# Optimization experiments

Hardware: AMD Instinct MI355X
Metric: run time of the kernel (lower is better)

Reference implementation:

```python
import jax, jax.numpy as jnp
import numpy as np

H_DIM = 2048
D_FF = 4 * H_DIM
NUM_EXPERTS = 8
NUM_SHARED = 2
BATCH, SEQ = 2, 2048


def setup_inputs() -> dict:
    key = jax.random.key(0)
    ks = jax.random.split(key, 10)
    s = 0.02
    return {
        "x": jax.random.normal(ks[0], (BATCH, SEQ, H_DIM), dtype=jnp.float32),
        "ws_w1": jax.random.normal(ks[1], (NUM_SHARED, H_DIM, D_FF), dtype=jnp.float32) * s,
        "ws_b1": jnp.zeros((NUM_SHARED, D_FF), dtype=jnp.float32),
        "ws_w2": jax.random.normal(ks[2], (NUM_SHARED, D_FF, H_DIM), dtype=jnp.float32) * s,
        "ws_b2": jnp.zeros((NUM_SHARED, H_DIM), dtype=jnp.float32),
        "we_w1": jax.random.normal(ks[3], (NUM_EXPERTS, H_DIM, D_FF), dtype=jnp.float32) * s,
        "we_b1": jnp.zeros((NUM_EXPERTS, D_FF), dtype=jnp.float32),
        "we_w2": jax.random.normal(ks[4], (NUM_EXPERTS, D_FF, H_DIM), dtype=jnp.float32) * s,
        "we_b2": jnp.zeros((NUM_EXPERTS, H_DIM), dtype=jnp.float32),
        "wg": jax.random.normal(ks[5], (H_DIM, NUM_EXPERTS), dtype=jnp.float32) * s,
        "top_k": 2,
    }


def reference(x, ws_w1, ws_b1, ws_w2, ws_b2, we_w1, we_b1, we_w2, we_b2, wg, top_k):
    B, S, D = x.shape
    xt = x.reshape(-1, D)  # [T, D], T = B*S
    T = xt.shape[0]

    # ---- shared experts: sum over NUM_SHARED dense MLPs ----
    hs = jax.nn.relu(jnp.einsum('td,ndf->ntf', xt, ws_w1) + ws_b1[:, None, :])
    shared = jnp.einsum('ntf,nfd->td', hs, ws_w2) + ws_b2.sum(axis=0)  # [T, D]

    # ---- sparse top-k routed MoE ----
    logits = xt @ wg                       # [T, E] router logits
    probs = jax.nn.softmax(logits, axis=-1)
    topv, topi = jax.lax.top_k(probs, top_k)
    gates = jnp.zeros_like(probs).at[jnp.arange(T)[:, None], topi].set(topv)  # [T, E]

    moe = jnp.zeros_like(xt)
    for e in range(we_w1.shape[0]):  # small fixed expert count
        he = jax.nn.relu(xt @ we_w1[e] + we_b1[e])
        ye = he @ we_w2[e] + we_b2[e]
        moe = moe + gates[:, e:e + 1] * ye

    out = (shared + moe).reshape(B, S, D)
    return out, logits
```

## Files before the change

### kernel.cpp

```cpp
#include <hip/hip_runtime.h>

#define TOKENS 4096
#define HD 2048
#define FF 8192
#define NE 8
#define NS 2

typedef __attribute__((ext_vector_type(8))) short bf16x8;
typedef __attribute__((ext_vector_type(4))) float f32x4;

__device__ __forceinline__ unsigned rnd_bf(unsigned u) {
  return u + 0x7fffu + ((u >> 16) & 1u);
}
__device__ __forceinline__ unsigned short f2bf(float f) {
  unsigned u = __builtin_bit_cast(unsigned, f);
  return (unsigned short)(rnd_bf(u) >> 16);
}

#define GLDS16(gp, lp)                                                         \
  __builtin_amdgcn_global_load_lds(                                            \
      (const __attribute__((address_space(1))) unsigned*)(const void*)(gp),    \
      (__attribute__((address_space(3))) unsigned*)(lp), 16, 0, 0)

__global__ void router_kernel(const float* __restrict__ x, const float* __restrict__ wg,
                              float* __restrict__ logits_out, int* __restrict__ topi,
                              float* __restrict__ topv, int* __restrict__ counts,
                              unsigned short* __restrict__ xb) {
  const int wave = threadIdx.x >> 6, lane = threadIdx.x & 63;
  const int t = blockIdx.x * 4 + wave;
  const float* xr = x + (size_t)t * HD;
  unsigned short* xbr = xb + (size_t)t * HD;
  float acc[8];
#pragma unroll
  for (int e = 0; e < 8; ++e) acc[e] = 0.f;
  for (int d = lane; d < HD; d += 64) {
    const float xv = xr[d];
    xbr[d] = f2bf(xv);
    const float4 w0 = *(const float4*)(wg + (size_t)d * 8);
    const float4 w1 = *(const float4*)(wg + (size_t)d * 8 + 4);
    acc[0] += xv * w0.x; acc[1] += xv * w0.y; acc[2] += xv * w0.z; acc[3] += xv * w0.w;
    acc[4] += xv * w1.x; acc[5] += xv * w1.y; acc[6] += xv * w1.z; acc[7] += xv * w1.w;
  }
#pragma unroll
  for (int e = 0; e < 8; ++e) {
#pragma unroll
    for (int off = 32; off > 0; off >>= 1) acc[e] += __shfl_xor(acc[e], off);
  }
  if (lane == 0) {
    *(float4*)(logits_out + (size_t)t * 8)     = make_float4(acc[0], acc[1], acc[2], acc[3]);
    *(float4*)(logits_out + (size_t)t * 8 + 4) = make_float4(acc[4], acc[5], acc[6], acc[7]);
    float mx = acc[0];
#pragma unroll
    for (int e = 1; e < 8; ++e) mx = fmaxf(mx, acc[e]);
    float p[8], s = 0.f;
#pragma unroll
    for (int e = 0; e < 8; ++e) { p[e] = expf(acc[e] - mx); s += p[e]; }
    const float inv = 1.f / s;
    int i1 = 0;
#pragma unroll
    for (int e = 1; e < 8; ++e) if (acc[e] > acc[i1]) i1 = e;
    int i2 = (i1 == 0) ? 1 : 0;
#pragma unroll
    for (int e = 0; e < 8; ++e) if (e != i1 && acc[e] > acc[i2]) i2 = e;
    topi[2 * t]     = i1; topv[2 * t]     = p[i1] * inv;
    topi[2 * t + 1] = i2; topv[2 * t + 1] = p[i2] * inv;
    atomicAdd(&counts[i1], 1);
    atomicAdd(&counts[i2], 1);
  }
}

__global__ void offs_kernel(const int* __restrict__ counts, int* __restrict__ offs,
                            int* __restrict__ cursors) {
  if (threadIdx.x == 0) {
    int r = 0;
    for (int e = 0; e < NE; ++e) { offs[e] = r; cursors[e] = r; r += counts[e]; }
  }
}

__global__ void gather_kernel(const unsigned short* __restrict__ xb,
                              const int* __restrict__ topi, const float* __restrict__ topv,
                              int* __restrict__ cursors, unsigned short* __restrict__ xg,
                              int* __restrict__ row_token, float* __restrict__ row_gate,
                              int* __restrict__ row_of) {
  const int wave = threadIdx.x >> 6, lane = threadIdx.x & 63;
  const int t = blockIdx.x * 4 + wave;
  const uint4* src = (const uint4*)(xb + (size_t)t * HD);
#pragma unroll
  for (int j = 0; j < 2; ++j) {
    const int e = topi[2 * t + j];
    int pos = 0;
    if (lane == 0) {
      pos = atomicAdd(&cursors[e], 1);
      row_token[pos] = t;
      row_gate[pos] = topv[2 * t + j];
      row_of[2 * t + j] = pos;
    }
    pos = __shfl(pos, 0);
    uint4* dst = (uint4*)(xg + (size_t)pos * HD);
#pragma unroll
    for (int c = lane; c < 256; c += 64) dst[c] = src[c];
  }
}

template <int K, int N>
__global__ __launch_bounds__(256) void pack_wt(const float* __restrict__ we,
                                               const float* __restrict__ ws,
                                               unsigned short* __restrict__ dstw) {
  const int e = blockIdx.z;
  const float* src = (e < NE) ? (we + (size_t)e * K * N) : (ws + (size_t)(e - NE) * K * N);
  unsigned short* dst = dstw + (size_t)e * K * N;
  const int nt = blockIdx.x * 64;
  const int kt = blockIdx.y * 64;
  __shared__ unsigned short t[64][73];
  const int tid = threadIdx.x;
  const int rr = tid >> 4, cc = (tid & 15) * 4;
#pragma unroll
  for (int i = 0; i < 4; ++i) {
    const int k = rr + i * 16;
    float4 v = *(const float4*)(src + (size_t)(kt + k) * N + nt + cc);
    t[k][cc + 0] = f2bf(v.x);
    t[k][cc + 1] = f2bf(v.y);
    t[k][cc + 2] = f2bf(v.z);
    t[k][cc + 3] = f2bf(v.w);
  }
  __syncthreads();
  const int nr = tid >> 2, kc = (tid & 3) * 16;
  unsigned u[8];
#pragma unroll
  for (int j = 0; j < 8; ++j)
    u[j] = (unsigned)t[kc + 2 * j][nr] | ((unsigned)t[kc + 2 * j + 1][nr] << 16);
  unsigned short* dp = dst + (size_t)(nt + nr) * K + kt + kc;
  uint4 v0; v0.x = u[0]; v0.y = u[1]; v0.z = u[2]; v0.w = u[3];
  uint4 v1; v1.x = u[4]; v1.y = u[5]; v1.z = u[6]; v1.w = u[7];
  *(uint4*)dp = v0;
  *(uint4*)(dp + 8) = v1;
}

template <int MS>
__device__ __forceinline__ void rd_a(bf16x8 (&d)[8], const unsigned short* base,
                                     int wr, int fr, int fq, int swz) {
#pragma unroll
  for (int mi = 0; mi < 4; ++mi)
#pragma unroll
    for (int ks = 0; ks < 2; ++ks)
      d[mi * 2 + ks] = *(const bf16x8*)(base + (wr * 128 + MS * 64 + mi * 16 + fr) * 64 +
                                        (((ks * 4 + fq) ^ swz) << 3));
}
template <int NSUB>
__device__ __forceinline__ void rd_b(bf16x8 (&d)[4], const unsigned short* base,
                                     int wc, int fr, int fq, int swz) {
#pragma unroll
  for (int ni = 0; ni < 2; ++ni)
#pragma unroll
    for (int ks = 0; ks < 2; ++ks)
      d[ni * 2 + ks] = *(const bf16x8*)(base + (wc * 64 + NSUB * 32 + ni * 16 + fr) * 64 +
                                        (((ks * 4 + fq) ^ swz) << 3));
}
template <int MS, int NSUB>
__device__ __forceinline__ void mm16(f32x4 (&acc)[8][4], const bf16x8 (&a)[8],
                                     const bf16x8 (&b)[4]) {
  __builtin_amdgcn_s_setprio(1);
#pragma unroll
  for (int mi = 0; mi < 4; ++mi)
#pragma unroll
    for (int ni = 0; ni < 2; ++ni)
#pragma unroll
      for (int ks = 0; ks < 2; ++ks)
        acc[MS * 4 + mi][NSUB * 2 + ni] = __builtin_amdgcn_mfma_f32_16x16x32_bf16(
            a[mi * 2 + ks], b[ni * 2 + ks], acc[MS * 4 + mi][NSUB * 2 + ni], 0, 0, 0);
  __builtin_amdgcn_s_setprio(0);
}

template <int K>
__device__ __forceinline__ void kloop(
    const unsigned short* __restrict__ A, const unsigned short* __restrict__ A2,
    const unsigned short* __restrict__ Bt, const unsigned short* __restrict__ Bt2,
    int ksw, unsigned short* smem, int m0, int n0, f32x4 (&acc)[8][4],
    int wr, int wc, int fr, int fq, int swz,
    int wrA, int wcB, int lr8, int lc8, int scol, int nkt) {
#define SAK(s, kt, b)                                                          \
  { int kl_ = (kt); const unsigned short* ab_ = A;                             \
    if (kl_ >= ksw) { ab_ = A2; kl_ -= ksw; }                                  \
    const int r0_ = wrA + (s) * 64 + lr8;                                      \
    const unsigned short* s_ = ab_ + (size_t)(m0 + r0_) * K + kl_ * 64 + scol; \
    unsigned short* d_ = smem + (b) * 32768 + r0_ * 64 + lc8 * 8;              \
    GLDS16(s_, d_); GLDS16(s_ + (size_t)8 * K, d_ + 8 * 64); }
#define SBK(s, kt, b)                                                          \
  { int kl_ = (kt); const unsigned short* bb_ = Bt;                            \
    if (kl_ >= ksw) { bb_ = Bt2; kl_ -= ksw; }                                 \
    const int r0_ = wcB + (s) * 32 + lr8;                                      \
    const unsigned short* s_ = bb_ + (size_t)(n0 + r0_) * K + kl_ * 64 + scol; \
    unsigned short* d_ = smem + (b) * 32768 + 16384 + r0_ * 64 + lc8 * 8;      \
    GLDS16(s_, d_); GLDS16(s_ + (size_t)8 * K, d_ + 8 * 64); }

  SAK(0, 0, 0); SAK(1, 0, 0); SBK(0, 0, 0); SBK(1, 0, 0);
  SAK(0, 1, 1); SAK(1, 1, 1); SBK(0, 1, 1); SBK(1, 1, 1);
  asm volatile("s_waitcnt vmcnt(8)" ::: "memory");
  __builtin_amdgcn_s_barrier();

  bf16x8 a0[8], a1[8], b0[4], b1[4];
  rd_a<0>(a0, smem, wr, fr, fq, swz);
  rd_b<0>(b0, smem + 16384, wc, fr, fq, swz);

  for (int t = 0; t < nkt; ++t) {
    const int cur = t & 1;
    const int tp2 = (t + 2 < nkt) ? t + 2 : t;
    const unsigned short* As_c = smem + cur * 32768;
    const unsigned short* Bs_c = As_c + 16384;
    const unsigned short* As_n = smem + (cur ^ 1) * 32768;
    const unsigned short* Bs_n = As_n + 16384;
    rd_b<1>(b1, Bs_c, wc, fr, fq, swz);
    mm16<0, 0>(acc, a0, b0);
    rd_a<1>(a1, As_c, wr, fr, fq, swz);
    mm16<0, 1>(acc, a0, b1);
    asm volatile("s_waitcnt lgkmcnt(0)" ::: "memory");
    __builtin_amdgcn_s_barrier();
    __builtin_amdgcn_sched_barrier(0);
    SAK(0, tp2, cur); SBK(0, tp2, cur);
    mm16<1, 0>(acc, a1, b0);
    asm volatile("s_waitcnt vmcnt(4)" ::: "memory");
    __builtin_amdgcn_s_barrier();
    __builtin_amdgcn_sched_barrier(0);
    rd_a<0>(a0, As_n, wr, fr, fq, swz);
    rd_b<0>(b0, Bs_n, wc, fr, fq, swz);
    SAK(1, tp2, cur); SBK(1, tp2, cur);
    mm16<1, 1>(acc, a1, b1);
  }
#undef SAK
#undef SBK
}

__global__ __launch_bounds__(512, 2) void g1k(
    const unsigned short* __restrict__ Ash, const unsigned short* __restrict__ Art,
    const unsigned short* __restrict__ wt1,
    const float* __restrict__ bE, const float* __restrict__ bS,
    unsigned short* __restrict__ hout,
    const int* __restrict__ counts, const int* __restrict__ offs,
    int do_pack, const float* __restrict__ we_w2, const float* __restrict__ ws_w2,
    unsigned short* __restrict__ wt2) {
  constexpr int K = HD;
  constexpr int NBX = FF / 256;
  constexpr int NWG = NBX * 16;
  extern __shared__ unsigned short smem[];

  const int e = blockIdx.z;
  int M;
  const unsigned short* A;
  const float* bias;
  int hbase;
  if (e < NE) {
    M = counts[e];
    A = Art + (size_t)offs[e] * K;
    bias = bE + (size_t)e * FF;
    hbase = offs[e];
  } else {
    M = TOKENS;
    A = Ash;
    bias = bS + (size_t)(e - NE) * FF;
    hbase = 2 * TOKENS + (e - NE) * TOKENS;
  }
  const unsigned short* Bt = wt1 + (size_t)e * HD * FF;

  int flat = blockIdx.x + NBX * blockIdx.y;
  flat = (flat & 7) * (NWG >> 3) + (flat >> 3);
  const int m0 = (flat & 15) * 256;
  const int n0 = (flat >> 4) * 256;
  const int tid = threadIdx.x;

  if (m0 >= M) {
    if (!do_pack) return;
    int total = 0, prefix = 0;
    for (int e2 = 0; e2 < NE; ++e2) {
      int mb = (counts[e2] + 255) >> 8; if (mb > 16) mb = 16;
      const int inv = 32 * (16 - mb);
      if (e2 < e) prefix += inv;
      total += inv;
    }
    int mb_e = (counts[e] + 255) >> 8; if (mb_e > 16) mb_e = 16;
    const int m_idx = flat & 15, n_idx = flat >> 4;
    const int rank = prefix + n_idx * (16 - mb_e) + (m_idx - mb_e);
    unsigned short* ps = smem;
    const int NT = 10 * 128 * 32;
    const int kk = tid >> 3, cc = (tid & 7) * 8;
    float4 r0a, r0b;
    int i = rank;
    if (i < NT) {
      const int e2 = i >> 12, rem = i & 4095, ktt = rem >> 5, ntt = rem & 31;
      const float* src = (e2 < NE) ? (we_w2 + (size_t)e2 * FF * HD)
                                   : (ws_w2 + (size_t)(e2 - NE) * FF * HD);
      const float* sp = src + (size_t)(ktt * 64 + kk) * HD + ntt * 64 + cc;
      r0a = *(const float4*)sp; r0b = *(const float4*)(sp + 4);
    }
    int it = 0;
    while (i < NT) {
      const int inext = i + total;
      float4 r1a, r1b;
      if (inext < NT) {
        const int e2 = inext >> 12, rem = inext & 4095, ktt = rem >> 5, ntt = rem & 31;
        const float* src = (e2 < NE) ? (we_w2 + (size_t)e2 * FF * HD)
                                     : (ws_w2 + (size_t)(e2 - NE) * FF * HD);
        const float* sp = src + (size_t)(ktt * 64 + kk) * HD + ntt * 64 + cc;
        r1a = *(const float4*)sp; r1b = *(const float4*)(sp + 4);
      }
      unsigned short* pb = ps + (it & 1) * (64 * 73);
      {
        unsigned short* tp = pb + kk * 73 + cc;
        tp[0] = f2bf(r0a.x); tp[1] = f2bf(r0a.y); tp[2] = f2bf(r0a.z); tp[3] = f2bf(r0a.w);
        tp[4] = f2bf(r0b.x); tp[5] = f2bf(r0b.y); tp[6] = f2bf(r0b.z); tp[7] = f2bf(r0b.w);
      }
      __syncthreads();
      {
        const int e2 = i >> 12, rem = i & 4095, ktt = rem >> 5, ntt = rem & 31;
        unsigned short* dst = wt2 + (size_t)e2 * HD * FF;
        const int nn = tid >> 3, kc = (tid & 7) * 8;
        unsigned u[4];
#pragma unroll
        for (int j = 0; j < 4; ++j)
          u[j] = (unsigned)pb[(kc + 2 * j) * 73 + nn] |
                 ((unsigned)pb[(kc + 2 * j + 1) * 73 + nn] << 16);
        uint4 v; v.x = u[0]; v.y = u[1]; v.z = u[2]; v.w = u[3];
        *(uint4*)(dst + (size_t)(ntt * 64 + nn) * FF + ktt * 64 + kc) = v;
      }
      r0a = r1a; r0b = r1b;
      i = inext; ++it;
    }
    return;
  }

  const int wid = tid >> 6, ln = tid & 63;
  const int wr = wid >> 2, wc = wid & 3;
  const int fr = ln & 15, fq = ln >> 4;
  const int swz = fr & 7;
  const int lr8 = ln >> 3;
  const int lc8 = ln & 7;
  const int scol = (lc8 ^ lr8) << 3;
  const int wrA = wr * 128 + wc * 16;
  const int wcB = wc * 64 + wr * 16;

  f32x4 acc[8][4];
#pragma unroll
  for (int i = 0; i < 8; ++i)
#pragma unroll
    for (int j = 0; j < 4; ++j) acc[i][j] = (f32x4){0.f, 0.f, 0.f, 0.f};

  kloop<K>(A, A, Bt, Bt, 1 << 30, smem, m0, n0, acc, wr, wc, fr, fq, swz,
           wrA, wcB, lr8, lc8, scol, K / 64);

#pragma unroll
  for (int nn = 0; nn < 4; ++nn) {
#pragma unroll
    for (int mm = 0; mm < 8; ++mm) {
      const int col = n0 + wc * 64 + (nn >> 1) * 32 + (nn & 1) * 16 + fr;
      const float bb = bias[col];
#pragma unroll
      for (int j = 0; j < 4; ++j) {
        const int r = m0 + wr * 128 + (mm >> 2) * 64 + (mm & 3) * 16 + fq * 4 + j;
        if (r < M) {
          float v = acc[mm][nn][j] + bb;
          v = v > 0.f ? v : 0.f;
          hout[(size_t)(hbase + r) * FF + col] = f2bf(v);
        }
      }
    }
  }
}

__global__ __launch_bounds__(512, 2) void g2k(
    const unsigned short* __restrict__ hbuf, const unsigned short* __restrict__ wt2,
    const float* __restrict__ bE, const float* __restrict__ bS,
    float* __restrict__ ybuf,
    const int* __restrict__ counts, const int* __restrict__ offs) {
  constexpr int K = FF;
  constexpr int NBX = HD / 256;
  constexpr int NWG = NBX * 16;
  extern __shared__ unsigned short smem[];

  const int e = blockIdx.z;
  const bool merged = (e == NE);
  int M, nkt, ksw, hbase;
  const unsigned short *A, *A2, *B, *B2;
  const float *bias, *bias2;
  if (!merged) {
    M = counts[e];
    A = hbuf + (size_t)offs[e] * K;  A2 = A;
    B = wt2 + (size_t)e * HD * FF;   B2 = B;
    bias = bE + (size_t)e * HD;      bias2 = nullptr;
    hbase = offs[e];
    nkt = 128; ksw = 1 << 30;
  } else {
    M = TOKENS;
    A  = hbuf + (size_t)(2 * TOKENS) * K;
    A2 = hbuf + (size_t)(3 * TOKENS) * K;
    B  = wt2 + (size_t)NE * HD * FF;
    B2 = wt2 + (size_t)(NE + 1) * HD * FF;
    bias = bS;  bias2 = bS + HD;
    hbase = 2 * TOKENS;
    nkt = 256; ksw = 128;
  }

  int flat = blockIdx.x + NBX * blockIdx.y;
  flat = (flat & 7) * (NWG >> 3) + (flat >> 3);
  const int m0 = (flat & 15) * 256;
  const int n0 = (flat >> 4) * 256;
  if (m0 >= M) return;

  const int tid = threadIdx.x;
  const int wid = tid >> 6, ln = tid & 63;
  const int wr = wid >> 2, wc = wid & 3;
  const int fr = ln & 15, fq = ln >> 4;
  const int swz = fr & 7;
  const int lr8 = ln >> 3;
  const int lc8 = ln & 7;
  const int scol = (lc8 ^ lr8) << 3;
  const int wrA = wr * 128 + wc * 16;
  const int wcB = wc * 64 + wr * 16;

  f32x4 acc[8][4];
#pragma unroll
  for (int i = 0; i < 8; ++i)
#pragma unroll
    for (int j = 0; j < 4; ++j) acc[i][j] = (f32x4){0.f, 0.f, 0.f, 0.f};

  kloop<K>(A, A2, B, B2, ksw, smem, m0, n0, acc, wr, wc, fr, fq, swz,
           wrA, wcB, lr8, lc8, scol, nkt);

#pragma unroll
  for (int nn = 0; nn < 4; ++nn) {
#pragma unroll
    for (int mm = 0; mm < 8; ++mm) {
      const int colw = wc * 64 + (nn >> 1) * 32 + (nn & 1) * 16 + fr;
      float bb = bias[n0 + colw];
      if (merged) bb += bias2[n0 + colw];
#pragma unroll
      for (int j = 0; j < 4; ++j) {
        const int r = m0 + wr * 128 + (mm >> 2) * 64 + (mm & 3) * 16 + fq * 4 + j;
        if (r < M)
          ybuf[(size_t)(hbase + r) * HD + n0 + colw] = acc[mm][nn][j] + bb;
      }
    }
  }
}

__global__ __launch_bounds__(256) void reduce_kernel(
    const float* __restrict__ ybuf, const int* __restrict__ row_of,
    const float* __restrict__ topv, float* __restrict__ out) {
  const int t = blockIdx.x;
  const int d = threadIdx.x * 8;
  const float g0 = topv[2 * t], g1 = topv[2 * t + 1];
  const float* y0 = ybuf + (size_t)row_of[2 * t] * HD + d;
  const float* y1 = ybuf + (size_t)row_of[2 * t + 1] * HD + d;
  const float* s0 = ybuf + (size_t)(2 * TOKENS + t) * HD + d;
  float* o = out + (size_t)t * HD + d;
#pragma unroll
  for (int q = 0; q < 2; ++q) {
    const float4 a = *(const float4*)(s0 + q * 4);
    const float4 c = *(const float4*)(y0 + q * 4);
    const float4 e = *(const float4*)(y1 + q * 4);
    float4 r;
    r.x = a.x + g0 * c.x + g1 * e.x;
    r.y = a.y + g0 * c.y + g1 * e.y;
    r.z = a.z + g0 * c.z + g1 * e.z;
    r.w = a.w + g0 * c.w + g1 * e.w;
    *(float4*)(o + q * 4) = r;
  }
}

extern "C" void kernel_launch(void* const* d_in, const int* in_sizes, int n_in,
                              void* d_out, int out_size, void* d_ws, size_t ws_size,
                              hipStream_t stream) {
  const float* x     = (const float*)d_in[0];
  const float* ws_w1 = (const float*)d_in[1];
  const float* ws_b1 = (const float*)d_in[2];
  const float* ws_w2 = (const float*)d_in[3];
  const float* ws_b2 = (const float*)d_in[4];
  const float* we_w1 = (const float*)d_in[5];
  const float* we_b1 = (const float*)d_in[6];
  const float* we_w2 = (const float*)d_in[7];
  const float* we_b2 = (const float*)d_in[8];
  const float* wg    = (const float*)d_in[9];

  float* out = (float*)d_out;
  float* logits = out + (size_t)TOKENS * HD;

  hipFuncSetAttribute(reinterpret_cast<const void*>(g1k),
                      hipFuncAttributeMaxDynamicSharedMemorySize, 131072);
  hipFuncSetAttribute(reinterpret_cast<const void*>(g2k),
                      hipFuncAttributeMaxDynamicSharedMemorySize, 131072);

  char* ws = (char*)d_ws;
  unsigned short* wt1  = (unsigned short*)ws;
  unsigned short* wt2  = (unsigned short*)(ws + 335544320);
  unsigned short* xb   = (unsigned short*)(ws + 671088640);
  unsigned short* xg   = (unsigned short*)(ws + 687865856);
  unsigned short* hbuf = (unsigned short*)(ws + 721944576);
  char* ctrl = ws + 990380032;
  float* ybuf = (float*)ws;
  int*   row_token = (int*)(ctrl);
  float* row_gate  = (float*)(ctrl + 32768);
  int*   topi      = (int*)(ctrl + 65536);
  float* topv      = (float*)(ctrl + 98304);
  int*   counts    = (int*)(ctrl + 131072);
  int*   offs      = (int*)(ctrl + 131104);
  int*   cursors   = (int*)(ctrl + 131136);
  int*   row_of    = (int*)(ctrl + 131168);

  hipMemsetAsync(counts, 0, NE * sizeof(int), stream);
  router_kernel<<<1024, 256, 0, stream>>>(x, wg, logits, topi, topv, counts, xb);
  offs_kernel<<<1, 64, 0, stream>>>(counts, offs, cursors);
  gather_kernel<<<1024, 256, 0, stream>>>(xb, topi, topv, cursors, xg,
                                          row_token, row_gate, row_of);
  pack_wt<HD, FF><<<dim3(FF / 64, HD / 64, 10), 256, 0, stream>>>(we_w1, ws_w1, wt1);
  g1k<<<dim3(32, 16, 10), 512, 131072, stream>>>(
      xb, xg, wt1, we_b1, ws_b1, hbuf, counts, offs, 1, we_w2, ws_w2, wt2);
  g2k<<<dim3(8, 16, 9), 512, 131072, stream>>>(
      hbuf, wt2, we_b2, ws_b2, ybuf, counts, offs);
  reduce_kernel<<<TOKENS, 256, 0, stream>>>(ybuf, row_of, topv, out);

  (void)in_sizes; (void)n_in; (void)out_size; (void)ws_size;
}
```

Measured before the change: 1.861 ms.

## Restructure GEMM k-loop into 8-phase ping-pong schedule with per-phase barriers

Replaces the double-buffered k-loop with an unrolled two-tile, eight-phase schedule. Each MFMA cluster is bracketed by workgroup barriers, and the LDS reads and global-to-LDS loads are interleaved between phases so that the waves alternate compute and memory work. The aim is to hide LDS and global load latency behind MFMA, in the style of a ping-pong between the two waves per SIMD. It adds many more barriers and tighter waitcnt accounting, and it assumes nkt is even.

```diff
diff --git a/kernel.cpp b/kernel.cpp
--- a/kernel.cpp
+++ b/kernel.cpp
@@ -171,8 +171,17 @@
   __builtin_amdgcn_s_setprio(0);
 }
 
+#define PH_BAR_PRE()                                                           \
+  __builtin_amdgcn_sched_barrier(0);                                           \
+  __builtin_amdgcn_s_barrier();                                                \
+  asm volatile("s_waitcnt lgkmcnt(0)" ::: "memory");                           \
+  __builtin_amdgcn_sched_barrier(0)
+#define PH_BAR_POST()                                                          \
+  __builtin_amdgcn_sched_barrier(0);                                           \
+  __builtin_amdgcn_s_barrier()
+
 template <int K>
-__device__ __forceinline__ void kloop(
+__device__ __forceinline__ void kloop8(
     const unsigned short* __restrict__ A, const unsigned short* __restrict__ A2,
     const unsigned short* __restrict__ Bt, const unsigned short* __restrict__ Bt2,
     int ksw, unsigned short* smem, int m0, int n0, f32x4 (&acc)[8][4],
@@ -193,39 +202,72 @@
     unsigned short* d_ = smem + (b) * 32768 + 16384 + r0_ * 64 + lc8 * 8;      \
     GLDS16(s_, d_); GLDS16(s_ + (size_t)8 * K, d_ + 8 * 64); }
 
-  SAK(0, 0, 0); SAK(1, 0, 0); SBK(0, 0, 0); SBK(1, 0, 0);
-  SAK(0, 1, 1); SAK(1, 1, 1); SBK(0, 1, 1); SBK(1, 1, 1);
-  asm volatile("s_waitcnt vmcnt(8)" ::: "memory");
+  SAK(0, 0, 0); SBK(0, 0, 0); SBK(1, 0, 0); SAK(1, 0, 0);
+  SAK(0, 1, 1); SBK(0, 1, 1); SBK(1, 1, 1);
+  asm volatile("s_waitcnt vmcnt(6)" ::: "memory");
   __builtin_amdgcn_s_barrier();
 
   bf16x8 a0[8], a1[8], b0[4], b1[4];
-  rd_a<0>(a0, smem, wr, fr, fq, swz);
-  rd_b<0>(b0, smem + 16384, wc, fr, fq, swz);
-
-  for (int t = 0; t < nkt; ++t) {
-    const int cur = t & 1;
-    const int tp2 = (t + 2 < nkt) ? t + 2 : t;
-    const unsigned short* As_c = smem + cur * 32768;
-    const unsigned short* Bs_c = As_c + 16384;
-    const unsigned short* As_n = smem + (cur ^ 1) * 32768;
-    const unsigned short* Bs_n = As_n + 16384;
-    rd_b<1>(b1, Bs_c, wc, fr, fq, swz);
+  const unsigned short* B0A = smem;
+  const unsigned short* B0B = smem + 16384;
+  const unsigned short* B1A = smem + 32768;
+  const unsigned short* B1B = smem + 49152;
+
+  const int half = nkt >> 1;
+  for (int i = 0; i < half; ++i) {
+    const int u = 2 * i, v = 2 * i + 1;
+    const int up2 = (u + 2 < nkt) ? u + 2 : u;
+    const int vp2 = (v + 2 < nkt) ? v + 2 : v;
+    rd_a<0>(a0, B0A, wr, fr, fq, swz);
+    rd_b<0>(b0, B0B, wc, fr, fq, swz);
+    SAK(1, v, 1);
+    asm volatile("s_waitcnt lgkmcnt(8)" ::: "memory");
+    PH_BAR_PRE();
     mm16<0, 0>(acc, a0, b0);
-    rd_a<1>(a1, As_c, wr, fr, fq, swz);
+    PH_BAR_POST();
+    rd_b<1>(b1, B0B, wc, fr, fq, swz);
+    SAK(0, up2, 0);
+    PH_BAR_PRE();
     mm16<0, 1>(acc, a0, b1);
-    asm volatile("s_waitcnt lgkmcnt(0)" ::: "memory");
+    PH_BAR_POST();
+    rd_a<1>(a1, B0A, wr, fr, fq, swz);
+    SBK(0, up2, 0);
+    PH_BAR_PRE();
+    mm16<1, 1>(acc, a1, b1);
+    PH_BAR_POST();
+    SBK(1, up2, 0);
+    asm volatile("s_waitcnt vmcnt(6)" ::: "memory");
+    __builtin_amdgcn_sched_barrier(0);
     __builtin_amdgcn_s_barrier();
     __builtin_amdgcn_sched_barrier(0);
-    SAK(0, tp2, cur); SBK(0, tp2, cur);
     mm16<1, 0>(acc, a1, b0);
-    asm volatile("s_waitcnt vmcnt(4)" ::: "memory");
+    PH_BAR_POST();
+    rd_a<0>(a0, B1A, wr, fr, fq, swz);
+    rd_b<0>(b0, B1B, wc, fr, fq, swz);
+    SAK(1, up2, 0);
+    asm volatile("s_waitcnt lgkmcnt(8)" ::: "memory");
+    PH_BAR_PRE();
+    mm16<0, 0>(acc, a0, b0);
+    PH_BAR_POST();
+    rd_b<1>(b1, B1B, wc, fr, fq, swz);
+    SAK(0, vp2, 1);
+    PH_BAR_PRE();
+    mm16<0, 1>(acc, a0, b1);
+    PH_BAR_POST();
+    rd_a<1>(a1, B1A, wr, fr, fq, swz);
+    SBK(0, vp2, 1);
+    PH_BAR_PRE();
+    mm16<1, 1>(acc, a1, b1);
+    PH_BAR_POST();
+    SBK(1, vp2, 1);
+    asm volatile("s_waitcnt vmcnt(6)" ::: "memory");
+    __builtin_amdgcn_sched_barrier(0);
     __builtin_amdgcn_s_barrier();
     __builtin_amdgcn_sched_barrier(0);
-    rd_a<0>(a0, As_n, wr, fr, fq, swz);
-    rd_b<0>(b0, Bs_n, wc, fr, fq, swz);
-    SAK(1, tp2, cur); SBK(1, tp2, cur);
-    mm16<1, 1>(acc, a1, b1);
-  }
+    mm16<1, 0>(acc, a1, b0);
+    PH_BAR_POST();
+  }
+  asm volatile("s_waitcnt vmcnt(0)" ::: "memory");
 #undef SAK
 #undef SBK
 }
@@ -343,8 +385,8 @@
 #pragma unroll
     for (int j = 0; j < 4; ++j) acc[i][j] = (f32x4){0.f, 0.f, 0.f, 0.f};
 
-  kloop<K>(A, A, Bt, Bt, 1 << 30, smem, m0, n0, acc, wr, wc, fr, fq, swz,
-           wrA, wcB, lr8, lc8, scol, K / 64);
+  kloop8<K>(A, A, Bt, Bt, 1 << 30, smem, m0, n0, acc, wr, wc, fr, fq, swz,
+            wrA, wcB, lr8, lc8, scol, K / 64);
 
 #pragma unroll
   for (int nn = 0; nn < 4; ++nn) {
@@ -421,8 +463,8 @@
 #pragma unroll
     for (int j = 0; j < 4; ++j) acc[i][j] = (f32x4){0.f, 0.f, 0.f, 0.f};
 
-  kloop<K>(A, A2, B, B2, ksw, smem, m0, n0, acc, wr, wc, fr, fq, swz,
-           wrA, wcB, lr8, lc8, scol, nkt);
+  kloop8<K>(A, A2, B, B2, ksw, smem, m0, n0, acc, wr, wc, fr, fq, swz,
+            wrA, wcB, lr8, lc8, scol, nkt);
 
 #pragma unroll
   for (int nn = 0; nn < 4; ++nn) {
```

After: 1.870 ms. About the same (+0.5%).
